# Optimization experiments

Measured on AMD Instinct MI355X. Metric: run time of the kernel, lower is better.

## Reference

```python
import jax, jax.numpy as jnp
import numpy as np

P, L, H = 3, 4, 6          # window size, num scales, num heads
EPS = 1e-5                 # LayerNorm eps (PyTorch default)


def setup_inputs() -> dict:
    key = jax.random.key(0)
    B, T, D = 8, 4096, 768
    ks = jax.random.split(key, 12)
    s = 0.02
    w = lambda k, shape: (jax.random.normal(k, shape, jnp.float32) * s)
    z = lambda n: jnp.zeros((n,), jnp.float32)
    return {
        "x": jax.random.normal(ks[0], (B, T, D), jnp.float32),
        "ln_g": jnp.ones((D,), jnp.float32),
        "ln_b": z(D),
        "qw": w(ks[1], (D, D)), "qb": z(D),
        "kw": w(ks[2], (D, D)), "kb": z(D),
        "vw": w(ks[3], (D, D)), "vb": z(D),
        "inw": w(ks[4], (3 * D, D)), "inb": z(3 * D),   # MHA in_proj
        "mow": w(ks[5], (D, D)), "mob": z(D),            # MHA out_proj
        "ow": w(ks[6], (D, D)), "ob": z(D),              # output_proj
    }


def _layernorm(x, g, b):
    mu = jnp.mean(x, -1, keepdims=True)
    var = jnp.mean((x - mu) ** 2, -1, keepdims=True)
    return (x - mu) * jax.lax.rsqrt(var + EPS) * g + b


def _mha_windows(q, k, v, inw, inb, mow, mob):
    # q,k,v: [B, W, P, D] -- batched tiny attention over all windows at once
    B, W, Pw, D = q.shape
    hd = D // H
    wq, wk, wv = inw[:D], inw[D:2 * D], inw[2 * D:]
    bq, bk, bv = inb[:D], inb[D:2 * D], inb[2 * D:]
    qp = (q @ wq.T + bq).reshape(B, W, Pw, H, hd)
    kp = (k @ wk.T + bk).reshape(B, W, Pw, H, hd)
    vp = (v @ wv.T + bv).reshape(B, W, Pw, H, hd)
    scores = jnp.einsum('bwqhd,bwkhd->bwhqk', qp, kp) / jnp.sqrt(jnp.float32(hd))
    attn = jax.nn.softmax(scores, axis=-1)
    o = jnp.einsum('bwhqk,bwkhd->bwqhd', attn, vp).reshape(B, W, Pw, D)
    return o @ mow.T + mob


def reference(x, ln_g, ln_b, qw, qb, kw, kb, vw, vb, inw, inb, mow, mob, ow, ob):
    B, T, D = x.shape
    xn = _layernorm(x, ln_g, ln_b)
    Q = xn @ qw.T + qb
    K = xn @ kw.T + kb
    V = xn @ vw.T + vb
    acc = jnp.zeros_like(x)
    for kk in range(L):
        scale = P ** kk
        if T < scale:
            continue
        Lp = T // scale
        pool = lambda z: z[:, :Lp * scale].reshape(B, Lp, scale, D).mean(axis=2)
        pQ, pK, pV = pool(Q), pool(K), pool(V)
        W = Lp // P
        if W == 0:
            continue
        win = lambda z: z[:, :W * P].reshape(B, W, P, D)
        o = _mha_windows(win(pQ), win(pK), win(pV), inw, inb, mow, mob)
        so = o.reshape(B, W * P, D)                       # concat of windows
        idx = (jnp.arange(T) * (W * P)) // T              # nearest interp to T
        up = so[:, idx]
        acc = acc + jax.nn.gelu(up, approximate=False)    # exact GELU (torch default)
    out = acc @ ow.T + ob
    return x + out
```

## Files before the change

kernel.cpp:

```cpp
#include <hip/hip_runtime.h>
#include <stdint.h>

typedef short s16x8 __attribute__((ext_vector_type(8)));
typedef float f32x4 __attribute__((ext_vector_type(4)));

__device__ __forceinline__ unsigned short f2bf(float f) {
  unsigned u = __builtin_bit_cast(unsigned, f);
  u = (u + 0x7FFFu + ((u >> 16) & 1u)) >> 16;
  return (unsigned short)u;
}
__device__ __forceinline__ float bf2f(unsigned short h) {
  unsigned u = ((unsigned)h) << 16;
  return __builtin_bit_cast(float, u);
}

__device__ __forceinline__ void gload_lds16(const void* g, void* l) {
  __builtin_amdgcn_global_load_lds((__attribute__((address_space(1))) void*)g,
                                   (__attribute__((address_space(3))) void*)l,
                                   16, 0, 0);
}

__global__ __launch_bounds__(256)
void mstr_convw(const float* __restrict__ inw, const float* __restrict__ mow,
                const float* __restrict__ ow, unsigned short* __restrict__ inwB,
                unsigned short* __restrict__ mowB, unsigned short* __restrict__ owB)
{
  long i = (long)blockIdx.x * 256 + threadIdx.x;
  const long n1 = 589824;
  if (i < 3 * n1)      inwB[i] = f2bf(inw[i]);
  else if (i < 4 * n1) mowB[i - 3 * n1] = f2bf(mow[i - 3 * n1]);
  else                 owB[i - 4 * n1] = f2bf(ow[i - 4 * n1]);
}

__global__ __launch_bounds__(256)
void mstr_transpose(const float* __restrict__ qw, const float* __restrict__ kw,
                    const float* __restrict__ vw, unsigned short* __restrict__ wT)
{
  const float* src = (blockIdx.z == 0) ? qw : (blockIdx.z == 1) ? kw : vw;
  unsigned short* dst = wT + (long)blockIdx.z * 589824;
  __shared__ float tile[32][33];
  int tx = threadIdx.x & 31, ty = threadIdx.x >> 5;
  int j0 = blockIdx.x * 32, k0 = blockIdx.y * 32;
#pragma unroll
  for (int i = 0; i < 4; ++i)
    tile[ty + i * 8][tx] = src[(long)(j0 + ty + i * 8) * 768 + k0 + tx];
  __syncthreads();
#pragma unroll
  for (int i = 0; i < 4; ++i)
    dst[(long)(k0 + ty + i * 8) * 768 + j0 + tx] = f2bf(tile[tx][ty + i * 8]);
}

__global__ __launch_bounds__(256)
void mstr_biascomb(const float* __restrict__ inw, const float* __restrict__ inb,
                   const float* __restrict__ qb, const float* __restrict__ kb,
                   const float* __restrict__ vb, float* __restrict__ bc,
                   float* __restrict__ zb)
{
  int gid = blockIdx.x * 256 + threadIdx.x;
  if (gid < 768) zb[gid] = 0.f;
  int s = gid / 768, c = gid - s * 768;
  const float* b = (s == 0) ? qb : (s == 1) ? kb : vb;
  const float* wrow = inw + (long)(s * 768 + c) * 768;
  float a = inb[s * 768 + c];
  for (int j = 0; j < 768; ++j) a += b[j] * wrow[j];
  bc[gid] = a;
}

__global__ __launch_bounds__(256)
void mstr_ln(const float* __restrict__ x, const float* __restrict__ g,
             const float* __restrict__ bt, unsigned short* __restrict__ xn)
{
  int blk = blockIdx.x;
  int bb = blk / 4095, t = blk - bb * 4095;
  const float* xr = x + ((long)bb * 4096 + t) * 768;
  unsigned short* orow = xn + (long)blk * 768;
  int tid = threadIdx.x;
  float v0 = xr[tid], v1 = xr[tid + 256], v2 = xr[tid + 512];
  float s = v0 + v1 + v2;
  float s2 = v0 * v0 + v1 * v1 + v2 * v2;
#pragma unroll
  for (int o = 32; o > 0; o >>= 1) { s += __shfl_down(s, o, 64); s2 += __shfl_down(s2, o, 64); }
  __shared__ float rs[4], rq[4];
  int lane = tid & 63, wid = tid >> 6;
  if (lane == 0) { rs[wid] = s; rq[wid] = s2; }
  __syncthreads();
  float S = rs[0] + rs[1] + rs[2] + rs[3];
  float S2 = rq[0] + rq[1] + rq[2] + rq[3];
  float mu = S * (1.0f / 768.0f);
  float var = S2 * (1.0f / 768.0f) - mu * mu;
  float rstd = rsqrtf(var + 1e-5f);
  orow[tid] = f2bf((v0 - mu) * rstd * g[tid] + bt[tid]);
  orow[tid + 256] = f2bf((v1 - mu) * rstd * g[tid + 256] + bt[tid + 256]);
  orow[tid + 512] = f2bf((v2 - mu) * rstd * g[tid + 512] + bt[tid + 512]);
}

template<int EPI>
__global__ __launch_bounds__(256, 2)
void mstr_gemm(const unsigned short* __restrict__ A, int M,
               const unsigned short* __restrict__ W,
               const float* __restrict__ bias,
               unsigned short* out0, unsigned short* out1, unsigned short* out2,
               float* outf, const float* xadd,
               int rowDiv, int rowStride, int NC, int nwg)
{
  __shared__ char smem[65536];
  int orig = blockIdx.x;
  int swq = nwg >> 3, swr = nwg & 7;
  int xcd = orig & 7, sidx = orig >> 3;
  int wg = (xcd < swr ? xcd * (swq + 1) : swr * (swq + 1) + (xcd - swr) * swq) + sidx;
  int rowp = wg / NC, colp = wg - rowp * NC;

  const int tid = threadIdx.x;
  const int lane = tid & 63;
  const int wid = tid >> 6;
  const int wr = wid >> 1, wc = wid & 1;
  const long row0 = (long)rowp * 128;
  const int col0 = colp * 128;

  const int sr = tid >> 2;
  const int sc = (((tid & 3) ^ ((tid >> 3) & 3)) << 3);
  long a0r = row0 + sr;       if (a0r >= M) a0r = M - 1;
  long a1r = row0 + sr + 64;  if (a1r >= M) a1r = M - 1;
  const unsigned short* Ag0 = A + a0r * 768 + sc;
  const unsigned short* Ag1 = A + a1r * 768 + sc;
  const unsigned short* Bg0 = W + (long)(col0 + sr) * 768 + sc;
  const unsigned short* Bg1 = W + (long)(col0 + sr + 64) * 768 + sc;
  char* ldsT = smem + tid * 16;

  const int fr = lane & 15;
  const int g4 = lane >> 4;
  const int cx = ((g4 ^ ((fr >> 1) & 3)) << 4);
  const int aoff = (wr * 64 + fr) * 64 + cx;
  const int boff = 8192 + (wc * 64 + fr) * 64 + cx;

  f32x4 acc[4][4] = {};

#define MSTAGE(T) { int kk_ = (T) * 32; int bo_ = ((T) & 3) * 16384; \
    gload_lds16(Ag0 + kk_, ldsT + bo_); \
    gload_lds16(Ag1 + kk_, ldsT + bo_ + 4096); \
    gload_lds16(Bg0 + kk_, ldsT + bo_ + 8192); \
    gload_lds16(Bg1 + kk_, ldsT + bo_ + 12288); }

  MSTAGE(0) MSTAGE(1) MSTAGE(2)
  asm volatile("s_waitcnt vmcnt(8)" ::: "memory");
  __builtin_amdgcn_s_barrier();

  for (int t = 0; t < 24; ++t) {
    if (t < 21) MSTAGE(t + 3)
    const int bo = (t & 3) * 16384;
    s16x8 af[4], bfv[4];
#pragma unroll
    for (int m = 0; m < 4; ++m) af[m] = *(const s16x8*)(smem + bo + aoff + m * 1024);
#pragma unroll
    for (int n = 0; n < 4; ++n) bfv[n] = *(const s16x8*)(smem + bo + boff + n * 1024);
    __builtin_amdgcn_s_setprio(1);
#pragma unroll
    for (int m = 0; m < 4; ++m)
#pragma unroll
      for (int n = 0; n < 4; ++n)
        acc[m][n] = __builtin_amdgcn_mfma_f32_16x16x32_bf16(af[m], bfv[n], acc[m][n], 0, 0, 0);
    __builtin_amdgcn_s_setprio(0);
    if (t < 23) {
      if (t < 21)       asm volatile("s_waitcnt vmcnt(8)" ::: "memory");
      else if (t == 21) asm volatile("s_waitcnt vmcnt(4)" ::: "memory");
      else              asm volatile("s_waitcnt vmcnt(0)" ::: "memory");
      __builtin_amdgcn_s_barrier();
    }
  }
#undef MSTAGE

  int seg = (col0 >= 1536) ? 2 : (col0 >= 768 ? 1 : 0);
  unsigned short* outp = (seg == 0) ? out0 : (seg == 1) ? out1 : out2;
  int csub = seg * 768;
#pragma unroll
  for (int m = 0; m < 4; ++m) {
#pragma unroll
    for (int r = 0; r < 4; ++r) {
      long gr = row0 + wr * 64 + m * 16 + g4 * 4 + r;
      if (gr < M) {
        long orow;
        if (EPI == 1) {
          orow = gr;
        } else {
          int qq = (int)gr / rowDiv;
          orow = (long)qq * rowStride + ((int)gr - qq * rowDiv);
        }
#pragma unroll
        for (int n = 0; n < 4; ++n) {
          int c = col0 + wc * 64 + n * 16 + fr;
          float v = acc[m][n][r] + bias[c];
          if (EPI == 1) {
            long o = gr * 768 + c;
            outf[o] = v + xadd[o];
          } else if (EPI == 2) {
            v = 0.5f * v * (1.0f + erff(v * 0.70710678118654752f));
            outp[orow * 768 + (c - csub)] = f2bf(v);
          } else {
            outp[orow * 768 + (c - csub)] = f2bf(v);
          }
        }
      }
    }
  }
}

__global__ __launch_bounds__(384)
void mstr_pool(unsigned short* qp, unsigned short* kp, unsigned short* vp,
               int srcOff, int dstOff, int Ndst)
{
  unsigned short* p = (blockIdx.y == 0) ? qp : (blockIdx.y == 1) ? kp : vp;
  int tok = blockIdx.x;
  int bb = tok / Ndst, j = tok - bb * Ndst;
  long sb = ((long)bb * 6063 + srcOff + 3 * j) * 768 + threadIdx.x * 2;
  long db = ((long)bb * 6063 + dstOff + j) * 768 + threadIdx.x * 2;
  unsigned a = *(const unsigned*)(p + sb);
  unsigned b = *(const unsigned*)(p + sb + 768);
  unsigned c = *(const unsigned*)(p + sb + 1536);
  float lo = (bf2f((unsigned short)a) + bf2f((unsigned short)b) + bf2f((unsigned short)c)) * (1.0f / 3.0f);
  float hi = (bf2f((unsigned short)(a >> 16)) + bf2f((unsigned short)(b >> 16)) + bf2f((unsigned short)(c >> 16))) * (1.0f / 3.0f);
  unsigned o = (unsigned)f2bf(lo) | ((unsigned)f2bf(hi) << 16);
  *(unsigned*)(p + db) = o;
}

__global__ __launch_bounds__(256)
void mstr_attn(unsigned short* qp, unsigned short* kp, unsigned short* vp, int nwaves)
{
  int gw = blockIdx.x * 4 + (threadIdx.x >> 6);
  if (gw >= nwaves) return;
  int lane = threadIdx.x & 63;
  int win = gw / 6, h = gw - win * 6;
  int bb = win / 2021, ww = win - bb * 2021;
  int row0;
  if (ww < 1365)      row0 = 3 * ww;
  else if (ww < 1820) row0 = 4095 + 3 * (ww - 1365);
  else if (ww < 1971) row0 = 5460 + 3 * (ww - 1820);
  else                row0 = 5913 + 3 * (ww - 1971);
  long base = ((long)bb * 6063 + row0) * 768 + h * 128 + lane * 2;
  float q[3][2], k[3][2], v[3][2];
#pragma unroll
  for (int i = 0; i < 3; ++i) {
    unsigned uq = *(const unsigned*)(qp + base + i * 768);
    unsigned uk = *(const unsigned*)(kp + base + i * 768);
    unsigned uv = *(const unsigned*)(vp + base + i * 768);
    q[i][0] = bf2f((unsigned short)uq); q[i][1] = bf2f((unsigned short)(uq >> 16));
    k[i][0] = bf2f((unsigned short)uk); k[i][1] = bf2f((unsigned short)(uk >> 16));
    v[i][0] = bf2f((unsigned short)uv); v[i][1] = bf2f((unsigned short)(uv >> 16));
  }
  float s[3][3];
#pragma unroll
  for (int i = 0; i < 3; ++i)
#pragma unroll
    for (int j = 0; j < 3; ++j)
      s[i][j] = q[i][0] * k[j][0] + q[i][1] * k[j][1];
#pragma unroll
  for (int st = 1; st < 64; st <<= 1) {
#pragma unroll
    for (int i = 0; i < 3; ++i)
#pragma unroll
      for (int j = 0; j < 3; ++j)
        s[i][j] += __shfl_xor(s[i][j], st, 64);
  }
  const float scl = 0.088388347648318447f;
#pragma unroll
  for (int i = 0; i < 3; ++i) {
    float s0 = s[i][0] * scl, s1 = s[i][1] * scl, s2 = s[i][2] * scl;
    float m = fmaxf(s0, fmaxf(s1, s2));
    float e0 = __expf(s0 - m), e1 = __expf(s1 - m), e2 = __expf(s2 - m);
    float inv = 1.0f / (e0 + e1 + e2);
    e0 *= inv; e1 *= inv; e2 *= inv;
    float o0 = e0 * v[0][0] + e1 * v[1][0] + e2 * v[2][0];
    float o1 = e0 * v[0][1] + e1 * v[1][1] + e2 * v[2][1];
    unsigned o = (unsigned)f2bf(o0) | ((unsigned)f2bf(o1) << 16);
    *(unsigned*)(qp + base + i * 768) = o;
  }
}

__global__ __launch_bounds__(256)
void mstr_gelusum(const unsigned short* __restrict__ omo, unsigned short* __restrict__ acc)
{
  long gid = (long)blockIdx.x * 256 + threadIdx.x;
  int d2 = (int)(gid % 384);
  long row = gid / 384;
  int bb = (int)(row >> 12);
  int t = (int)(row & 4095);
  const int NkA[4] = {4095, 1365, 453, 150};
  const int soA[4] = {0, 4095, 5460, 5913};
  float a0 = 0.f, a1 = 0.f;
#pragma unroll
  for (int kk = 0; kk < 4; ++kk) {
    int idx = (t * NkA[kk]) >> 12;
    long tok = (long)bb * 6063 + soA[kk] + idx;
    unsigned u = *(const unsigned*)(omo + tok * 768 + d2 * 2);
    a0 += bf2f((unsigned short)u);
    a1 += bf2f((unsigned short)(u >> 16));
  }
  unsigned o = (unsigned)f2bf(a0) | ((unsigned)f2bf(a1) << 16);
  *(unsigned*)(acc + row * 768 + d2 * 2) = o;
}

extern "C" void kernel_launch(void* const* d_in, const int* in_sizes, int n_in,
                              void* d_out, int out_size, void* d_ws, size_t ws_size,
                              hipStream_t stream)
{
  const float* x   = (const float*)d_in[0];
  const float* lng = (const float*)d_in[1];
  const float* lnb = (const float*)d_in[2];
  const float* qw  = (const float*)d_in[3];
  const float* qb  = (const float*)d_in[4];
  const float* kw  = (const float*)d_in[5];
  const float* kb  = (const float*)d_in[6];
  const float* vw  = (const float*)d_in[7];
  const float* vb  = (const float*)d_in[8];
  const float* inw = (const float*)d_in[9];
  const float* inb = (const float*)d_in[10];
  const float* mob = (const float*)d_in[12];
  const float* ow  = (const float*)d_in[13];
  const float* ob  = (const float*)d_in[14];

  const long n1 = 589824;
  char* ws = (char*)d_ws;
  size_t off = 0;
  auto alloc = [&](size_t bytes) -> char* {
    char* p = ws + off;
    off += (bytes + 255) & ~(size_t)255;
    return p;
  };
  unsigned short* Wc = (unsigned short*)alloc((size_t)5 * n1 * 2);
  float* bc = (float*)alloc(2304 * 4);
  float* zb = (float*)alloc(768 * 4);
  size_t fixed = off;

  int g = 0;
  const int cands[4] = {8, 4, 2, 1};
  for (int ci = 0; ci < 4; ++ci) {
    int c = cands[ci];
    size_t need = fixed + (size_t)c * 4096 * 768 * 2
                + 2 * (size_t)c * 6063 * 768 * 2
                + 1024;
    if (need <= ws_size) { g = c; break; }
  }
  if (!g) return;

  char* GR = ws + fixed;
  unsigned short* xnacc = (unsigned short*)GR;
  unsigned short* qp = xnacc + (size_t)g * 4096 * 768;
  unsigned short* kp = qp + (size_t)g * 6063 * 768;
  unsigned short* inwB = (unsigned short*)GR;
  unsigned short* wT   = inwB + 3 * n1;

  unsigned short* mowB = Wc + 3 * n1;
  unsigned short* owB  = Wc + 4 * n1;

  mstr_convw<<<dim3(11520), dim3(256), 0, stream>>>(inw, (const float*)d_in[11], ow, inwB, mowB, owB);
  mstr_transpose<<<dim3(24, 24, 3), dim3(256), 0, stream>>>(qw, kw, vw, wT);
  mstr_biascomb<<<dim3(9), dim3(256), 0, stream>>>(inw, inb, qb, kb, vb, bc, zb);
  for (int s = 0; s < 3; ++s)
    mstr_gemm<0><<<dim3(36), dim3(256), 0, stream>>>(inwB + (long)s * n1, 768, wT + (long)s * n1,
                                                     zb, Wc + (long)s * n1, Wc + (long)s * n1,
                                                     Wc + (long)s * n1, nullptr, nullptr, 768, 768, 6, 36);

  int ng = 8 / g;
  for (int gi = 0; gi < ng; ++gi) {
    const float* xg = x + (long)gi * g * 4096 * 768;
    unsigned short* vp = (unsigned short*)d_out + (long)gi * g * 4096 * 768 * 2;
    mstr_ln<<<dim3(g * 4095), dim3(256), 0, stream>>>(xg, lng, lnb, xnacc);
    int M1 = g * 4095, gb1 = (M1 + 127) / 128;
    int nwg1 = gb1 * 18;
    mstr_gemm<0><<<dim3(nwg1), dim3(256), 0, stream>>>(xnacc, M1, Wc, bc,
                                                       qp, kp, vp, nullptr, nullptr,
                                                       4095, 6063, 18, nwg1);
    mstr_pool<<<dim3(g * 1365, 3), dim3(384), 0, stream>>>(qp, kp, vp, 0, 4095, 1365);
    mstr_pool<<<dim3(g * 453, 3), dim3(384), 0, stream>>>(qp, kp, vp, 4095, 5460, 453);
    mstr_pool<<<dim3(g * 150, 3), dim3(384), 0, stream>>>(qp, kp, vp, 5460, 5913, 150);
    int nw = g * 2021 * 6;
    mstr_attn<<<dim3((nw + 3) / 4), dim3(256), 0, stream>>>(qp, kp, vp, nw);
    int M2 = g * 6063;
    int nwg2 = ((M2 + 127) / 128) * 6;
    mstr_gemm<2><<<dim3(nwg2), dim3(256), 0, stream>>>(qp, M2, mowB, mob, kp, kp, kp,
                                                       nullptr, nullptr, M2, 0, 6, nwg2);
    mstr_gelusum<<<dim3(g * 6144), dim3(256), 0, stream>>>(kp, xnacc);
    int M3 = g * 4096;
    int nwg3 = (M3 / 128) * 6;
    mstr_gemm<1><<<dim3(nwg3), dim3(256), 0, stream>>>(xnacc, M3, owB, ob, nullptr, nullptr, nullptr,
                                                       (float*)d_out + (long)gi * g * 4096 * 768, xg,
                                                       M3, 0, 6, nwg3);
  }
}
```

Baseline: 641.9 us.

## Enlarge GEMM tiles to 256x256 with 8 waves and double-buffered K=64 stages

Rewrites the bf16 MFMA GEMM to use 256x256 output tiles computed by 512 threads (8 waves, each 128x64). It uses 128 KB of LDS with two K=64 buffers and a new XOR swizzle, and issues the next stage's global-to-LDS loads partway through four compute phases per K step. The goal is more data reuse per loaded byte and fewer workgroups. The cost is more barriers per iteration, higher register pressure from 32 accumulators per thread, and far fewer workgroups for the small weight-fusion GEMMs (9 blocks), which could hurt occupancy and load balance.

After: 756.6 us. +17.9%, slower.

```diff
diff --git a/kernel.cpp b/kernel.cpp
--- a/kernel.cpp
+++ b/kernel.cpp
@@ -95,7 +95,7 @@
 }
 
 template<int EPI>
-__global__ __launch_bounds__(256, 2)
+__global__ __launch_bounds__(512, 2)
 void mstr_gemm(const unsigned short* __restrict__ A, int M,
                const unsigned short* __restrict__ W,
                const float* __restrict__ bias,
@@ -103,7 +103,7 @@
                float* outf, const float* xadd,
                int rowDiv, int rowStride, int NC, int nwg)
 {
-  __shared__ char smem[65536];
+  __shared__ char smem[131072];
   int orig = blockIdx.x;
   int swq = nwg >> 3, swr = nwg & 7;
   int xcd = orig & 7, sidx = orig >> 3;
@@ -113,70 +113,108 @@
   const int tid = threadIdx.x;
   const int lane = tid & 63;
   const int wid = tid >> 6;
-  const int wr = wid >> 1, wc = wid & 1;
-  const long row0 = (long)rowp * 128;
-  const int col0 = colp * 128;
-
-  const int sr = tid >> 2;
-  const int sc = (((tid & 3) ^ ((tid >> 3) & 3)) << 3);
-  long a0r = row0 + sr;       if (a0r >= M) a0r = M - 1;
-  long a1r = row0 + sr + 64;  if (a1r >= M) a1r = M - 1;
-  const unsigned short* Ag0 = A + a0r * 768 + sc;
-  const unsigned short* Ag1 = A + a1r * 768 + sc;
-  const unsigned short* Bg0 = W + (long)(col0 + sr) * 768 + sc;
-  const unsigned short* Bg1 = W + (long)(col0 + sr + 64) * 768 + sc;
-  char* ldsT = smem + tid * 16;
+  const int wr = wid >> 2;
+  const int wc = wid & 3;
+  const long row0 = (long)rowp * 256;
+  const int col0 = colp * 256;
+
+  const int L0 = tid * 16, L1 = tid * 16 + 8192;
+  const int S0 = L0 ^ (((L0 >> 9) & 1) << 5);
+  const int S1 = L1 ^ (((L1 >> 9) & 1) << 5);
+  const int r0 = S0 >> 7, c0 = (S0 & 127) >> 1;
+  const int r1 = S1 >> 7, c1 = (S1 & 127) >> 1;
+  long ar00 = row0 + r0;        if (ar00 >= M) ar00 = M - 1;
+  long ar01 = row0 + r1;        if (ar01 >= M) ar01 = M - 1;
+  long ar10 = row0 + 128 + r0;  if (ar10 >= M) ar10 = M - 1;
+  long ar11 = row0 + 128 + r1;  if (ar11 >= M) ar11 = M - 1;
+  const unsigned short* pa0 = A + ar00 * 768 + c0;
+  const unsigned short* pa1 = A + ar01 * 768 + c1;
+  const unsigned short* pa2 = A + ar10 * 768 + c0;
+  const unsigned short* pa3 = A + ar11 * 768 + c1;
+  const unsigned short* pb0 = W + (long)(col0 + r0) * 768 + c0;
+  const unsigned short* pb1 = W + (long)(col0 + r1) * 768 + c1;
+  const unsigned short* pb2 = W + (long)(col0 + 128 + r0) * 768 + c0;
+  const unsigned short* pb3 = W + (long)(col0 + 128 + r1) * 768 + c1;
 
   const int fr = lane & 15;
   const int g4 = lane >> 4;
-  const int cx = ((g4 ^ ((fr >> 1) & 3)) << 4);
-  const int aoff = (wr * 64 + fr) * 64 + cx;
-  const int boff = 8192 + (wc * 64 + fr) * 64 + cx;
-
-  f32x4 acc[4][4] = {};
-
-#define MSTAGE(T) { int kk_ = (T) * 32; int bo_ = ((T) & 3) * 16384; \
-    gload_lds16(Ag0 + kk_, ldsT + bo_); \
-    gload_lds16(Ag1 + kk_, ldsT + bo_ + 4096); \
-    gload_lds16(Bg0 + kk_, ldsT + bo_ + 8192); \
-    gload_lds16(Bg1 + kk_, ldsT + bo_ + 12288); }
-
-  MSTAGE(0) MSTAGE(1) MSTAGE(2)
-  asm volatile("s_waitcnt vmcnt(8)" ::: "memory");
+  const int gx = (g4 * 16) ^ (((fr >> 2) & 1) << 5);
+  const int abase = wr * 16384 + fr * 128 + gx;
+  const int bbase = 32768 + (wc >> 1) * 16384 + ((wc & 1) * 64 + fr) * 128 + gx;
+
+  f32x4 acc[8][4] = {};
+  s16x8 bfv[4];
+
+#define STAGE_A(KT, BASE) { \
+    gload_lds16(pa0 + (KT) * 64, smem + (BASE) + L0); \
+    gload_lds16(pa1 + (KT) * 64, smem + (BASE) + L1); \
+    gload_lds16(pa2 + (KT) * 64, smem + (BASE) + 16384 + L0); \
+    gload_lds16(pa3 + (KT) * 64, smem + (BASE) + 16384 + L1); }
+#define STAGE_B(KT, BASE) { \
+    gload_lds16(pb0 + (KT) * 64, smem + (BASE) + 32768 + L0); \
+    gload_lds16(pb1 + (KT) * 64, smem + (BASE) + 32768 + L1); \
+    gload_lds16(pb2 + (KT) * 64, smem + (BASE) + 49152 + L0); \
+    gload_lds16(pb3 + (KT) * 64, smem + (BASE) + 49152 + L1); }
+
+  STAGE_A(0, 0)
+  STAGE_B(0, 0)
+  asm volatile("s_waitcnt vmcnt(0)" ::: "memory");
   __builtin_amdgcn_s_barrier();
 
-  for (int t = 0; t < 24; ++t) {
-    if (t < 21) MSTAGE(t + 3)
-    const int bo = (t & 3) * 16384;
-    s16x8 af[4], bfv[4];
-#pragma unroll
-    for (int m = 0; m < 4; ++m) af[m] = *(const s16x8*)(smem + bo + aoff + m * 1024);
-#pragma unroll
-    for (int n = 0; n < 4; ++n) bfv[n] = *(const s16x8*)(smem + bo + boff + n * 1024);
-    __builtin_amdgcn_s_setprio(1);
-#pragma unroll
-    for (int m = 0; m < 4; ++m)
-#pragma unroll
-      for (int n = 0; n < 4; ++n)
-        acc[m][n] = __builtin_amdgcn_mfma_f32_16x16x32_bf16(af[m], bfv[n], acc[m][n], 0, 0, 0);
-    __builtin_amdgcn_s_setprio(0);
-    if (t < 23) {
-      if (t < 21)       asm volatile("s_waitcnt vmcnt(8)" ::: "memory");
-      else if (t == 21) asm volatile("s_waitcnt vmcnt(4)" ::: "memory");
-      else              asm volatile("s_waitcnt vmcnt(0)" ::: "memory");
-      __builtin_amdgcn_s_barrier();
-    }
-  }
-#undef MSTAGE
+  for (int kt = 0; kt < 12; ++kt) {
+    const int db = (kt & 1) << 16;
+    const int nb = ((kt & 1) ^ 1) << 16;
+    const bool pf = (kt < 11);
+
+#define PHASE(QK, QM, SA, SB) { \
+      s16x8 af[4]; \
+      const char* ab = smem + db + abase + (QK) * 64 + (QM) * 8192; \
+      af[0] = *(const s16x8*)(ab); \
+      af[1] = *(const s16x8*)(ab + 2048); \
+      af[2] = *(const s16x8*)(ab + 4096); \
+      af[3] = *(const s16x8*)(ab + 6144); \
+      if (QM == 0) { \
+        const char* bb = smem + db + bbase + (QK) * 64; \
+        bfv[0] = *(const s16x8*)(bb); \
+        bfv[1] = *(const s16x8*)(bb + 2048); \
+        bfv[2] = *(const s16x8*)(bb + 4096); \
+        bfv[3] = *(const s16x8*)(bb + 6144); \
+      } \
+      if (SA && pf) STAGE_A(kt + 1, nb) \
+      if (SB && pf) STAGE_B(kt + 1, nb) \
+      __builtin_amdgcn_s_barrier(); \
+      asm volatile("s_waitcnt lgkmcnt(0)" ::: "memory"); \
+      __builtin_amdgcn_sched_barrier(0); \
+      __builtin_amdgcn_s_setprio(1); \
+      _Pragma("unroll") \
+      for (int m = 0; m < 4; ++m) \
+        _Pragma("unroll") \
+        for (int n = 0; n < 4; ++n) \
+          acc[(QM) * 4 + m][n] = __builtin_amdgcn_mfma_f32_16x16x32_bf16(af[m], bfv[n], acc[(QM) * 4 + m][n], 0, 0, 0); \
+      __builtin_amdgcn_s_setprio(0); }
+
+    PHASE(0, 0, 1, 0)
+    __builtin_amdgcn_s_barrier();
+    PHASE(0, 1, 0, 1)
+    __builtin_amdgcn_s_barrier();
+    PHASE(1, 0, 0, 0)
+    __builtin_amdgcn_s_barrier();
+    PHASE(1, 1, 0, 0)
+    if (pf) asm volatile("s_waitcnt vmcnt(0)" ::: "memory");
+    __builtin_amdgcn_s_barrier();
+#undef PHASE
+  }
+#undef STAGE_A
+#undef STAGE_B
 
   int seg = (col0 >= 1536) ? 2 : (col0 >= 768 ? 1 : 0);
   unsigned short* outp = (seg == 0) ? out0 : (seg == 1) ? out1 : out2;
   int csub = seg * 768;
 #pragma unroll
-  for (int m = 0; m < 4; ++m) {
+  for (int m = 0; m < 8; ++m) {
 #pragma unroll
     for (int r = 0; r < 4; ++r) {
-      long gr = row0 + wr * 64 + m * 16 + g4 * 4 + r;
+      long gr = row0 + wr * 128 + m * 16 + g4 * 4 + r;
       if (gr < M) {
         long orow;
         if (EPI == 1) {
@@ -355,34 +393,34 @@
   mstr_transpose<<<dim3(24, 24, 3), dim3(256), 0, stream>>>(qw, kw, vw, wT);
   mstr_biascomb<<<dim3(9), dim3(256), 0, stream>>>(inw, inb, qb, kb, vb, bc, zb);
   for (int s = 0; s < 3; ++s)
-    mstr_gemm<0><<<dim3(36), dim3(256), 0, stream>>>(inwB + (long)s * n1, 768, wT + (long)s * n1,
-                                                     zb, Wc + (long)s * n1, Wc + (long)s * n1,
-                                                     Wc + (long)s * n1, nullptr, nullptr, 768, 768, 6, 36);
+    mstr_gemm<0><<<dim3(9), dim3(512), 0, stream>>>(inwB + (long)s * n1, 768, wT + (long)s * n1,
+                                                    zb, Wc + (long)s * n1, Wc + (long)s * n1,
+                                                    Wc + (long)s * n1, nullptr, nullptr, 768, 768, 3, 9);
 
   int ng = 8 / g;
   for (int gi = 0; gi < ng; ++gi) {
     const float* xg = x + (long)gi * g * 4096 * 768;
     unsigned short* vp = (unsigned short*)d_out + (long)gi * g * 4096 * 768 * 2;
     mstr_ln<<<dim3(g * 4095), dim3(256), 0, stream>>>(xg, lng, lnb, xnacc);
-    int M1 = g * 4095, gb1 = (M1 + 127) / 128;
-    int nwg1 = gb1 * 18;
-    mstr_gemm<0><<<dim3(nwg1), dim3(256), 0, stream>>>(xnacc, M1, Wc, bc,
+    int M1 = g * 4095, gb1 = (M1 + 255) / 256;
+    int nwg1 = gb1 * 9;
+    mstr_gemm<0><<<dim3(nwg1), dim3(512), 0, stream>>>(xnacc, M1, Wc, bc,
                                                        qp, kp, vp, nullptr, nullptr,
-                                                       4095, 6063, 18, nwg1);
+                                                       4095, 6063, 9, nwg1);
     mstr_pool<<<dim3(g * 1365, 3), dim3(384), 0, stream>>>(qp, kp, vp, 0, 4095, 1365);
     mstr_pool<<<dim3(g * 453, 3), dim3(384), 0, stream>>>(qp, kp, vp, 4095, 5460, 453);
     mstr_pool<<<dim3(g * 150, 3), dim3(384), 0, stream>>>(qp, kp, vp, 5460, 5913, 150);
     int nw = g * 2021 * 6;
     mstr_attn<<<dim3((nw + 3) / 4), dim3(256), 0, stream>>>(qp, kp, vp, nw);
     int M2 = g * 6063;
-    int nwg2 = ((M2 + 127) / 128) * 6;
-    mstr_gemm<2><<<dim3(nwg2), dim3(256), 0, stream>>>(qp, M2, mowB, mob, kp, kp, kp,
-                                                       nullptr, nullptr, M2, 0, 6, nwg2);
+    int nwg2 = ((M2 + 255) / 256) * 3;
+    mstr_gemm<2><<<dim3(nwg2), dim3(512), 0, stream>>>(qp, M2, mowB, mob, kp, kp, kp,
+                                                       nullptr, nullptr, M2, 0, 3, nwg2);
     mstr_gelusum<<<dim3(g * 6144), dim3(256), 0, stream>>>(kp, xnacc);
     int M3 = g * 4096;
-    int nwg3 = (M3 / 128) * 6;
-    mstr_gemm<1><<<dim3(nwg3), dim3(256), 0, stream>>>(xnacc, M3, owB, ob, nullptr, nullptr, nullptr,
+    int nwg3 = ((M3 + 255) / 256) * 3;
+    mstr_gemm<1><<<dim3(nwg3), dim3(512), 0, stream>>>(xnacc, M3, owB, ob, nullptr, nullptr, nullptr,
                                                        (float*)d_out + (long)gi * g * 4096 * 768, xg,
-                                                       M3, 0, 6, nwg3);
-  }
-}
+                                                       M3, 0, 3, nwg3);
+  }
+}
```
